# Kernel optimization log

Measured on AMD Instinct MI355X. Metric: run time of the kernel, lower is better.

## Reference

```python
import jax, jax.numpy as jnp
import numpy as np

B, S, D, H = 2, 4096, 128, 128
EPS = 1e-6
NEG_INF = -1e30


def _complex_linear(xr, xi, Wr, Wi, br, bi):
    # x: (B,S,D); W: (H,D); complex linear (Wr + i Wi)(xr + i xi) + (br + i bi) per layer math:
    # real_out = (xr Wr + br) - (xi Wi + bi); imag_out = (xi Wr + br) + (xr Wi + bi)
    out_r = xr @ Wr.T + br - (xi @ Wi.T + bi)
    out_i = xi @ Wr.T + br + (xr @ Wi.T + bi)
    return out_r, out_i


def setup_inputs() -> dict:
    key = jax.random.key(0)
    ks = jax.random.split(key, 24)
    scale = 1.0 / np.sqrt(D)
    def W(k):
        return jax.random.normal(k, (H, D), jnp.float32) * scale
    def b(k):
        return jax.random.normal(k, (H,), jnp.float32) * 0.01
    inp = {
        "Z_q": jax.random.normal(ks[0], (B, 2, S, D, 1), jnp.float32),
        "Z_k": jax.random.normal(ks[1], (B, 2, S, D, 1), jnp.float32),
        "Z_v": jax.random.normal(ks[2], (B, 2, S, D, 1), jnp.float32),
        "Wq_r": W(ks[3]), "Wq_i": W(ks[4]), "bq_r": b(ks[5]), "bq_i": b(ks[6]),
        "Wk_r": W(ks[7]), "Wk_i": W(ks[8]), "bk_r": b(ks[9]), "bk_i": b(ks[10]),
        "Wv_r": W(ks[11]), "Wv_i": W(ks[12]), "bv_r": b(ks[13]), "bv_i": b(ks[14]),
        "Wp_r": W(ks[15]), "Wp_i": W(ks[16]), "bp_r": b(ks[17]), "bp_i": b(ks[18]),
        "noise_floor": jnp.asarray(1.0, jnp.float32),
        "tau": jnp.asarray(0.0, jnp.float32),
    }
    return inp


def reference(Z_q, Z_k, Z_v,
              Wq_r, Wq_i, bq_r, bq_i,
              Wk_r, Wk_i, bk_r, bk_i,
              Wv_r, Wv_i, bv_r, bv_i,
              Wp_r, Wp_i, bp_r, bp_i,
              noise_floor, tau):
    # squeeze trailing singleton; split real/imag -> (B,S,D)
    zqr, zqi = Z_q[:, 0, :, :, 0], Z_q[:, 1, :, :, 0]
    zkr, zki = Z_k[:, 0, :, :, 0], Z_k[:, 1, :, :, 0]
    zvr, zvi = Z_v[:, 0, :, :, 0], Z_v[:, 1, :, :, 0]

    Qr, Qi = _complex_linear(zqr, zqi, Wq_r, Wq_i, bq_r, bq_i)
    Kr, Ki = _complex_linear(zkr, zki, Wk_r, Wk_i, bk_r, bk_i)
    Vr, Vi = _complex_linear(zvr, zvi, Wv_r, Wv_i, bv_r, bv_i)

    # InverseMahalanobis: R2[b,i,j] = sum_h |Q[b,i]-K[b,j]|^2
    q2 = jnp.sum(Qr * Qr + Qi * Qi, axis=-1)          # (B,S)
    k2 = jnp.sum(Kr * Kr + Ki * Ki, axis=-1)          # (B,S)
    re_qk = (jnp.einsum('bsh,bth->bst', Qr, Kr)
             + jnp.einsum('bsh,bth->bst', Qi, Ki))    # (B,S,S)
    R2 = q2[:, :, None] + k2[:, None, :] - 2.0 * re_qk

    attn_scores = -jax.nn.softplus(tau) * jnp.log(noise_floor ** 2 + R2 + EPS)
    mask = jnp.tril(jnp.ones((S, S), dtype=bool))[None]
    attn_scores = jnp.where(mask, attn_scores, NEG_INF)
    attn_weights = jax.nn.softmax(attn_scores / jnp.sqrt(jnp.float32(H)), axis=-1)

    # attn (real) times complex V
    est_r = jnp.einsum('bst,bth->bsh', attn_weights, Vr)
    est_i = jnp.einsum('bst,bth->bsh', attn_weights, Vi)

    out_r, out_i = _complex_linear(est_r, est_i, Wp_r, Wp_i, bp_r, bp_i)
    out = jnp.stack((out_r, out_i), axis=1)[..., None]  # (B,2,S,H,1)
    return out, attn_weights
```

## Files before the change

### kernel.cpp

```cpp
#include <hip/hip_runtime.h>

#define S_LEN 4096
#define OUT_ELEMS 2097152

typedef _Float16 f16;
typedef _Float16 f16x8 __attribute__((ext_vector_type(8)));
typedef _Float16 f16x4 __attribute__((ext_vector_type(4)));
typedef float f32x4 __attribute__((ext_vector_type(4)));

#define MT_OFF    0x000000
#define BIAS_OFF  0x080000
#define SC_OFF    0x081000
#define BVP_OFF   0x082000
#define W2_OFF    0x090000
#define QH_OFF    0x100000
#define KH_OFF    0x500000
#define Q2_OFF    0xD00000
#define K2_OFF    0xD10000
#define L_OFF     0xD20000
#define VPT_OFF   0xE00000
#define PW_OFF    0x1600000
#define WS_NEED   0x5600000

#define MFMA16(A,B,C) __builtin_amdgcn_mfma_f32_16x16x32_f16(A,B,C,0,0,0)

__device__ __forceinline__ void async_cp16(f16* lds, const f16* g) {
  __builtin_amdgcn_global_load_lds(
      (const __attribute__((address_space(1))) void*)g,
      (__attribute__((address_space(3))) void*)lds, 16, 0, 0);
}


__device__ __forceinline__ void stage16(f16* lds, const f16* g, int stride, int tid) {
#pragma unroll
  for (int i = 0; i < 2; ++i) {
    int idx = i*256 + tid;
    int row = idx >> 2, c = idx & 3;
    int cs = c ^ ((row >> 1) & 3);
    async_cp16(lds + idx*8, g + (size_t)row*stride + cs*8);
  }
}

__device__ __forceinline__ void stage32(f16* lds, const float* g, int stride, int tid) {
#pragma unroll
  for (int i = 0; i < 4; ++i) {
    int idx = i*256 + tid;
    int row = idx >> 3, c = idx & 7;
    const float4* gp = (const float4*)(g + (size_t)row*stride + c*4);
    float4 v = *gp;
    f16x4 h; h[0]=(f16)v.x; h[1]=(f16)v.y; h[2]=(f16)v.z; h[3]=(f16)v.w;
    int cl = (((c >> 1) ^ ((row >> 1) & 3)) << 1) | (c & 1);
    *(f16x4*)(lds + row*32 + cl*4) = h;
  }
}

__device__ __forceinline__ void mfma_step(const f16* Asm, const f16* Bsm, int lane,
                                          int wm, int wn, f32x4 acc[4][4]) {
  f16x8 a[4], b[4];
  int rr = lane & 15;
  int sc = (lane >> 4) ^ ((rr >> 1) & 3);
#pragma unroll
  for (int i=0;i<4;i++) a[i] = *(const f16x8*)(Asm + (wm + i*16 + rr)*32 + (sc<<3));
#pragma unroll
  for (int j=0;j<4;j++) b[j] = *(const f16x8*)(Bsm + (wn + j*16 + rr)*32 + (sc<<3));
#pragma unroll
  for (int i=0;i<4;i++)
#pragma unroll
    for (int j=0;j<4;j++) acc[i][j] = MFMA16(a[i], b[j], acc[i][j]);
}

__global__ __launch_bounds__(256)
void k_build(const float* Wqr, const float* Wqi, const float* bqr, const float* bqi,
             const float* Wkr, const float* Wki, const float* bkr, const float* bki,
             const float* Wvr, const float* Wvi, const float* bvr, const float* bvi,
             const float* Wpr, const float* Wpi, const float* bpr, const float* bpi,
             f16* Mt, float* bias) {
  int mat = blockIdx.x;
  const float *Wr, *Wi, *br, *bi;
  if (mat == 0)      { Wr=Wqr; Wi=Wqi; br=bqr; bi=bqi; }
  else if (mat == 1) { Wr=Wkr; Wi=Wki; br=bkr; bi=bki; }
  else if (mat == 2) { Wr=Wvr; Wi=Wvi; br=bvr; bi=bvi; }
  else               { Wr=Wpr; Wi=Wpi; br=bpr; bi=bpi; }
  int idx = blockIdx.y*256 + threadIdx.x;
  int n = idx >> 8, k = idx & 255;
  int d = k & 127, h = n & 127;
  float w = (k < 128) ? ((n < 128) ? Wr[h*128+d] : Wi[h*128+d])
                      : ((n < 128) ? -Wi[h*128+d] : Wr[h*128+d]);
  Mt[mat*65536 + n*256 + k] = (f16)w;
  if (k == 0)
    bias[mat*256 + n] = (n < 128) ? (br[n] - bi[n]) : (br[n-128] + bi[n-128]);
}

__global__ __launch_bounds__(256)
void k_build2(const f16* Mt, const float* bias, f16* W2t, float* bvp) {
  int n = blockIdx.x, k = threadIdx.x;
  const f16* Mtv = Mt + 2*65536;
  const f16* Mtp = Mt + 3*65536;
  float acc = 0.f;
  for (int j = 0; j < 256; ++j)
    acc += (float)Mtv[j*256 + k] * (float)Mtp[n*256 + j];
  W2t[n*256 + k] = (f16)acc;
  if (k == 0) {
    float a = 0.f;
    for (int j = 0; j < 256; ++j) a += bias[2*256 + j] * (float)Mtp[n*256 + j];
    bvp[n] = a;
  }
}

__global__ __launch_bounds__(256)
void k_init(float* outp, float* attn, float* zreg, float* sc, const float* bias,
            const float* nf, const float* tau) {
  int bx = blockIdx.x, tid = threadIdx.x;
  float4 z = make_float4(0.f,0.f,0.f,0.f);
  if (bx < 992) {
    int b = bx >= 496; int r = bx - b*496;
    int tb = 1; while (r >= tb) { r -= tb; tb++; }
    int sb = r;
    float* base = attn + ((size_t)(b*S_LEN) + sb*128)*S_LEN + tb*128;
    int c4 = tid & 31;
#pragma unroll
    for (int it = 0; it < 16; ++it) {
      int row = it*8 + (tid >> 5);
      *(float4*)(base + (size_t)row*S_LEN + c4*4) = z;
    }
    return;
  }
  int idx = (bx - 992)*256 + tid;
  if (idx < 524288) {
    int h4 = idx & 31;
    int comp = (idx >> 17) & 1;
    ((float4*)outp)[idx] = *(const float4*)(bias + 3*256 + comp*128 + h4*4);
  } else {
    int j = idx - 524288;
    if (j < 12288) ((float4*)zreg)[j] = z;
  }
  if (idx == 0) {
    float t = tau[0];
    float c = __builtin_log2f(1.0f + __builtin_exp2f(t * 1.4426950408889634f))
              * 0.6931471805599453f;
    sc[0] = -c * 0.08838834764831845f;
    sc[1] = nf[0]*nf[0] + 1e-6f;
  }
}

__global__ __launch_bounds__(256)
void k_proj(const float* Zq, const float* Zk, const float* Zv,
            const f16* Mt, const f16* W2t, const float* bias, const float* bvp,
            f16* Qh, f16* Kh, f16* VPt, float* q2, float* k2) {
  __shared__ f16 smem[17408];
  __shared__ float bias_s[128];
  f16* A0 = smem;
  f16* A1 = smem + 4096;
  f16* B0 = smem + 8192;
  f16* B1 = smem + 12288;
  int tid = threadIdx.x;
  int mode = blockIdx.z;
  int m0 = blockIdx.x * 128, n0 = blockIdx.y * 128;
  const float* Z = (mode==0) ? Zq : (mode==1 ? Zk : Zv);
  const f16* Bt = (mode==2) ? W2t : (Mt + mode*65536);
  if (tid < 128) bias_s[tid] = (mode==2) ? bvp[n0 + tid] : bias[mode*256 + n0 + tid];
  int b = m0 >> 12, s0 = m0 & 4095;
  int lane = tid & 63, w = tid >> 6;
  int wm = (w >> 1)*64, wn = (w & 1)*64;
  f32x4 acc[4][4] = {};
  {
    const float* Ag = Z + (((size_t)(b*2 + 0))*S_LEN + s0)*128 + 0;
    stage32(A0, Ag, 128, tid);
    stage16(B0, Bt + n0*256 + 0, 256, tid);
  }
  __syncthreads();
  for (int kb = 0; kb < 8; ++kb) {
    int cur = kb & 1;
    if (kb < 7) {
      int k1 = (kb+1)*32;
      int part = k1 >> 7, d0 = k1 & 127;
      const float* Ag = Z + (((size_t)(b*2 + part))*S_LEN + s0)*128 + d0;
      stage32(cur ? A0 : A1, Ag, 128, tid);
      stage16(cur ? B0 : B1, Bt + n0*256 + k1, 256, tid);
    }
    mfma_step(cur ? A1 : A0, cur ? B1 : B0, lane, wm, wn, acc);
    __syncthreads();
  }
  int rr2 = (lane>>4)*4, cc = lane & 15;
  f16* Osm = smem;
  float rs[4][4];
#pragma unroll
  for (int i=0;i<4;i++)
#pragma unroll
    for (int r=0;r<4;r++) rs[i][r]=0.f;
  if (mode < 2) {
#pragma unroll
    for (int i=0;i<4;i++)
#pragma unroll
      for (int j=0;j<4;j++) {
        int cl = wn + j*16 + cc;
        float bv = bias_s[cl];
#pragma unroll
        for (int r=0;r<4;r++) {
          int rl = wm + i*16 + rr2 + r;
          f16 hv = (f16)(acc[i][j][r] + bv);
          Osm[rl*136 + cl] = hv;
          float fv = (float)hv;
          rs[i][r] += fv*fv;
        }
      }
  } else {
#pragma unroll
    for (int i=0;i<4;i++)
#pragma unroll
      for (int j=0;j<4;j++) {
        int cl = wn + j*16 + cc;
        float bv = bias_s[cl];
#pragma unroll
        for (int r=0;r<4;r++) {
          int rl = wm + i*16 + rr2 + r;
          Osm[cl*136 + rl] = (f16)(acc[i][j][r] + bv);
        }
      }
  }
  __syncthreads();
  if (mode < 2) {
    f16* O = (mode==0) ? Qh : Kh;
#pragma unroll
    for (int i2 = 0; i2 < 8; ++i2) {
      int idx = i2*256 + tid;
      int row = idx >> 4, c = idx & 15;
      *(f16x8*)(O + (size_t)(m0+row)*256 + n0 + c*8) = *(const f16x8*)(Osm + row*136 + c*8);
    }
#pragma unroll
    for (int m=8;m>=1;m>>=1)
#pragma unroll
      for (int i=0;i<4;i++)
#pragma unroll
        for (int r=0;r<4;r++) rs[i][r] += __shfl_xor(rs[i][r], m, 64);
    if (cc == 0) {
      float* T = (mode==0) ? q2 : k2;
#pragma unroll
      for (int i=0;i<4;i++)
#pragma unroll
        for (int r=0;r<4;r++) {
          int rg = m0 + wm + i*16 + rr2 + r;
          atomicAdd(&T[rg], rs[i][r]);
        }
    }
  } else {
#pragma unroll
    for (int i2 = 0; i2 < 8; ++i2) {
      int idx = i2*256 + tid;
      int row = idx >> 4, c = idx & 15;
      *(f16x8*)(VPt + (size_t)b*1048576 + (size_t)(n0+row)*4096 + s0 + c*8)
          = *(const f16x8*)(Osm + row*136 + c*8);
    }
  }
}

__global__ __launch_bounds__(256)
void k_attn(const f16* Qh, const f16* Kh, const float* q2, const float* k2,
            const float* sc, float* lsum, f16* Pws) {
  __shared__ f16 smem[4*128*32];
  __shared__ float q2s[128], k2s[128];
  f16* Asm0 = smem;
  f16* Asm1 = smem + 4096;
  f16* Bsm0 = smem + 8192;
  f16* Bsm1 = smem + 12288;
  int x = blockIdx.x;
  int b = x >= 528; int r = x - b*528;
  int sb = 0; while (r > sb) { r -= sb + 1; sb++; }
  int tb = r;
  int s0 = sb*128, t0 = tb*128;
  int tid = threadIdx.x;
  if (tid < 128) {
    q2s[tid] = q2[b*S_LEN + s0 + tid];
    k2s[tid] = k2[b*S_LEN + t0 + tid];
  }
  float kc = sc[0], nf2 = sc[1];
  int lane = tid & 63, w = tid >> 6;
  int wm = (w >> 1)*64, wn = (w & 1)*64;
  const f16* Ag = Qh + ((size_t)(b*S_LEN) + s0)*256;
  const f16* Bg = Kh + ((size_t)(b*S_LEN) + t0)*256;
  f32x4 acc[4][4] = {};
  stage16(Asm0, Ag, 256, tid);
  stage16(Bsm0, Bg, 256, tid);
  __syncthreads();
  for (int kb=0;kb<8;kb++) {
    int cur = kb & 1;
    if (kb < 7) {
      stage16(cur ? Asm0 : Asm1, Ag + (kb+1)*32, 256, tid);
      stage16(cur ? Bsm0 : Bsm1, Bg + (kb+1)*32, 256, tid);
    }
    mfma_step(cur ? Asm1 : Asm0, cur ? Bsm1 : Bsm0, lane, wm, wn, acc);
    __syncthreads();
  }
  f16* Psm = smem;
  int rr = (lane>>4)*4, cc = lane & 15;
  bool diag = (tb == sb);
  float rs[4][4];
#pragma unroll
  for (int i=0;i<4;i++)
#pragma unroll
    for (int rg=0;rg<4;rg++) rs[i][rg]=0.f;
#pragma unroll
  for (int i=0;i<4;i++)
#pragma unroll
    for (int j=0;j<4;j++) {
      int cl = wn + j*16 + cc;
      float kv = k2s[cl];
#pragma unroll
      for (int rg=0;rg<4;rg++) {
        int rl = wm + i*16 + rr + rg;
        float xx = nf2 + q2s[rl] + kv - 2.0f*acc[i][j][rg];
        float P = __builtin_exp2f(kc * __builtin_log2f(__builtin_fmaxf(xx, 1e-6f)));
        if (diag && (t0+cl) > (s0+rl)) P = 0.f;
        Psm[rl*128 + cl] = (f16)P;
        rs[i][rg] += P;
      }
    }
  __syncthreads();
  f16* Pg = Pws + ((size_t)(b*S_LEN) + s0)*S_LEN + t0;
#pragma unroll
  for (int i2 = 0; i2 < 8; ++i2) {
    int idx = i2*256 + tid;
    int row = idx >> 4, c = idx & 15;
    *(f16x8*)(Pg + (size_t)row*S_LEN + c*8) = *(const f16x8*)(Psm + row*128 + c*8);
  }
#pragma unroll
  for (int m=8;m>=1;m>>=1)
#pragma unroll
    for (int i=0;i<4;i++)
#pragma unroll
      for (int rg=0;rg<4;rg++) rs[i][rg] += __shfl_xor(rs[i][rg], m, 64);
  if (cc == 0)
#pragma unroll
    for (int i=0;i<4;i++)
#pragma unroll
      for (int rg=0;rg<4;rg++) {
        int rl = wm + i*16 + rr + rg;
        atomicAdd(&lsum[b*S_LEN + s0 + rl], rs[i][rg]);
      }
}

__global__ __launch_bounds__(512)
void k_pv(const f16* Pws, const f16* VPt, const float* lsum, float* outp, float* attn) {
  __shared__ f16 Asm[2][128*32];
  __shared__ f16 Bsm[2][256*32];
  __shared__ float ls[128];
  int r = blockIdx.x, b = blockIdx.y;
  int sb = 0;
  while (r >= ((sb+4)>>2)) { r -= (sb+4)>>2; sb++; }
  int c = r;
  int s0 = sb*128;
  int tid = threadIdx.x;
  if (tid < 128) ls[tid] = 1.0f / lsum[b*S_LEN + s0 + tid];
  int lane = tid & 63, w = tid >> 6;
  int wm = (w>>2)*64, wn = (w&3)*64;
  int tb0 = c*4, tb1 = tb0 + 4; if (tb1 > sb+1) tb1 = sb+1;
  int nt = (tb1 - tb0) * 4;
  int base_t = tb0*128;
  const f16* Abase = Pws + ((size_t)(b*S_LEN) + s0)*S_LEN + base_t;
  const f16* Bbase = VPt + (size_t)b*1048576 + base_t;
  f32x4 acc[4][4] = {};
  {
    int row = tid >> 2, cc0 = tid & 3, cs = cc0 ^ ((row >> 1) & 3);
    async_cp16(Asm[0] + tid*8, Abase + (size_t)row*S_LEN + cs*8);
  }
#pragma unroll
  for (int i=0;i<2;i++) {
    int idx = i*512 + tid, row = idx >> 2, cc0 = idx & 3, cs = cc0 ^ ((row >> 1) & 3);
    async_cp16(Bsm[0] + idx*8, Bbase + (size_t)row*4096 + cs*8);
  }
  __syncthreads();
  for (int st = 0; st < nt; ++st) {
    int cur = st & 1;
    int tcur = base_t + st*32;
    if (st + 1 < nt) {
      const f16* Ag = Abase + (st+1)*32;
      const f16* Bg = Bbase + (st+1)*32;
      {
        int row = tid >> 2, cc0 = tid & 3, cs = cc0 ^ ((row >> 1) & 3);
        async_cp16(Asm[cur^1] + tid*8, Ag + (size_t)row*S_LEN + cs*8);
      }
#pragma unroll
      for (int i=0;i<2;i++) {
        int idx = i*512 + tid, row = idx >> 2, cc0 = idx & 3, cs = cc0 ^ ((row >> 1) & 3);
        async_cp16(Bsm[cur^1] + idx*8, Bg + (size_t)row*4096 + cs*8);
      }
    }
#pragma unroll
    for (int i2=0;i2<2;i2++) {
      int idx = i2*512 + tid, row = idx >> 3, c4 = idx & 7;
      int cs = (c4 >> 1) ^ ((row >> 1) & 3);
      f16x4 v = *(const f16x4*)(Asm[cur] + row*32 + cs*8 + (c4 & 1)*4);
      float invl = ls[row];
      float4 o;
      o.x=(float)v[0]*invl; o.y=(float)v[1]*invl;
      o.z=(float)v[2]*invl; o.w=(float)v[3]*invl;
      *(float4*)(attn + ((size_t)(b*S_LEN) + s0 + row)*S_LEN + tcur + c4*4) = o;
    }
    mfma_step(Asm[cur], Bsm[cur], lane, wm, wn, acc);
    __syncthreads();
  }
  int rr2 = (lane>>4)*4, cc = lane & 15;
#pragma unroll
  for (int i=0;i<4;i++)
#pragma unroll
    for (int j=0;j<4;j++) {
      int cg = wn + j*16 + cc;
      int comp = cg >> 7, h = cg & 127;
#pragma unroll
      for (int rg=0;rg<4;rg++) {
        int rl = wm + i*16 + rr2 + rg;
        float v = acc[i][j][rg] * ls[rl];
        atomicAdd(&outp[(((size_t)(b*2 + comp))*S_LEN + s0 + rl)*128 + h], v);
      }
    }
}

extern "C" void kernel_launch(void* const* d_in, const int* in_sizes, int n_in,
                              void* d_out, int out_size, void* d_ws, size_t ws_size,
                              hipStream_t stream) {
  (void)in_sizes; (void)n_in; (void)out_size;
  if (ws_size < (size_t)WS_NEED) return;
  const float* Zq = (const float*)d_in[0];
  const float* Zk = (const float*)d_in[1];
  const float* Zv = (const float*)d_in[2];
  char* ws = (char*)d_ws;
  f16*   Mt   = (f16*)(ws + MT_OFF);
  float* bias = (float*)(ws + BIAS_OFF);
  float* sc   = (float*)(ws + SC_OFF);
  float* bvp  = (float*)(ws + BVP_OFF);
  f16*   W2t  = (f16*)(ws + W2_OFF);
  f16*   Qh   = (f16*)(ws + QH_OFF);
  f16*   Kh   = (f16*)(ws + KH_OFF);
  float* q2   = (float*)(ws + Q2_OFF);
  float* k2   = (float*)(ws + K2_OFF);
  float* lsum = (float*)(ws + L_OFF);
  f16*   VPt  = (f16*)(ws + VPT_OFF);
  f16*   Pws  = (f16*)(ws + PW_OFF);
  float* outp = (float*)d_out;
  float* attn = outp + OUT_ELEMS;

  k_build<<<dim3(4,256), 256, 0, stream>>>(
      (const float*)d_in[3],  (const float*)d_in[4],  (const float*)d_in[5],  (const float*)d_in[6],
      (const float*)d_in[7],  (const float*)d_in[8],  (const float*)d_in[9],  (const float*)d_in[10],
      (const float*)d_in[11], (const float*)d_in[12], (const float*)d_in[13], (const float*)d_in[14],
      (const float*)d_in[15], (const float*)d_in[16], (const float*)d_in[17], (const float*)d_in[18],
      Mt, bias);
  k_build2<<<256, 256, 0, stream>>>(Mt, bias, W2t, bvp);
  k_init<<<3088, 256, 0, stream>>>(outp, attn, q2, sc, bias,
                                   (const float*)d_in[19], (const float*)d_in[20]);
  k_proj<<<dim3(64,2,3), 256, 0, stream>>>(Zq, Zk, Zv, Mt, W2t, bias, bvp,
                                           Qh, Kh, VPt, q2, k2);
  k_attn<<<1056, 256, 0, stream>>>(Qh, Kh, q2, k2, sc, lsum, Pws);
  k_pv<<<dim3(144,2), 512, 0, stream>>>(Pws, VPt, lsum, outp, attn);
}
```

Baseline: 303.2 us.

## Prefetch two stages ahead with explicit vmcnt waits in score and PV kernels

Both MFMA main loops now issue async global-to-LDS copies two k-steps ahead instead of one. __syncthreads is replaced by explicit s_waitcnt vmcnt counts, raw s_barrier calls and sched_barrier fences, so a load can remain in flight while the previous tile is consumed. The aim is to hide global memory latency behind MFMA work. The hand-counted vmcnt values depend on the exact number of memory instructions the compiler emits (including the attn stores in the PV loop), which risks races if the counts are wrong.

```diff
diff --git a/kernel.cpp b/kernel.cpp
--- a/kernel.cpp
+++ b/kernel.cpp
@@ -279,17 +279,26 @@
   const f16* Ag = Qh + ((size_t)(b*S_LEN) + s0)*256;
   const f16* Bg = Kh + ((size_t)(b*S_LEN) + t0)*256;
   f32x4 acc[4][4] = {};
-  stage16(Asm0, Ag, 256, tid);
-  stage16(Bsm0, Bg, 256, tid);
-  __syncthreads();
-  for (int kb=0;kb<8;kb++) {
-    int cur = kb & 1;
-    if (kb < 7) {
-      stage16(cur ? Asm0 : Asm1, Ag + (kb+1)*32, 256, tid);
-      stage16(cur ? Bsm0 : Bsm1, Bg + (kb+1)*32, 256, tid);
-    }
-    mfma_step(cur ? Asm1 : Asm0, cur ? Bsm1 : Bsm0, lane, wm, wn, acc);
-    __syncthreads();
+  stage16(Asm0, Ag,      256, tid);
+  stage16(Bsm0, Bg,      256, tid);
+  stage16(Asm1, Ag + 32, 256, tid);
+  stage16(Bsm1, Bg + 32, 256, tid);
+  for (int kb = 0; kb < 8; ++kb) {
+    if (kb == 0)      asm volatile("s_waitcnt vmcnt(4) lgkmcnt(0)" ::: "memory");
+    else if (kb == 7) asm volatile("s_waitcnt vmcnt(0)" ::: "memory");
+    else              asm volatile("s_waitcnt vmcnt(4)" ::: "memory");
+    __builtin_amdgcn_s_barrier();
+    __builtin_amdgcn_sched_barrier(0);
+    f16* Acur = (kb & 1) ? Asm1 : Asm0;
+    f16* Bcur = (kb & 1) ? Bsm1 : Bsm0;
+    mfma_step(Acur, Bcur, lane, wm, wn, acc);
+    __builtin_amdgcn_sched_barrier(0);
+    __builtin_amdgcn_s_barrier();
+    __builtin_amdgcn_sched_barrier(0);
+    if (kb < 6) {
+      stage16(Acur, Ag + (kb+2)*32, 256, tid);
+      stage16(Bcur, Bg + (kb+2)*32, 256, tid);
+    }
   }
   f16* Psm = smem;
   int rr = (lane>>4)*4, cc = lane & 15;
@@ -359,32 +368,24 @@
   const f16* Abase = Pws + ((size_t)(b*S_LEN) + s0)*S_LEN + base_t;
   const f16* Bbase = VPt + (size_t)b*1048576 + base_t;
   f32x4 acc[4][4] = {};
-  {
-    int row = tid >> 2, cc0 = tid & 3, cs = cc0 ^ ((row >> 1) & 3);
-    async_cp16(Asm[0] + tid*8, Abase + (size_t)row*S_LEN + cs*8);
-  }
-#pragma unroll
-  for (int i=0;i<2;i++) {
-    int idx = i*512 + tid, row = idx >> 2, cc0 = idx & 3, cs = cc0 ^ ((row >> 1) & 3);
-    async_cp16(Bsm[0] + idx*8, Bbase + (size_t)row*4096 + cs*8);
-  }
-  __syncthreads();
+  int rowA = tid >> 2, ccA = tid & 3, csA = ccA ^ ((rowA >> 1) & 3);
+#pragma unroll
+  for (int t = 0; t < 2; ++t) {
+    async_cp16(Asm[t] + tid*8, Abase + t*32 + (size_t)rowA*S_LEN + csA*8);
+#pragma unroll
+    for (int i=0;i<2;i++) {
+      int idx = i*512 + tid, row = idx >> 2, cc0 = idx & 3, cs = cc0 ^ ((row >> 1) & 3);
+      async_cp16(Bsm[t] + idx*8, Bbase + t*32 + (size_t)row*4096 + cs*8);
+    }
+  }
   for (int st = 0; st < nt; ++st) {
     int cur = st & 1;
     int tcur = base_t + st*32;
-    if (st + 1 < nt) {
-      const f16* Ag = Abase + (st+1)*32;
-      const f16* Bg = Bbase + (st+1)*32;
-      {
-        int row = tid >> 2, cc0 = tid & 3, cs = cc0 ^ ((row >> 1) & 3);
-        async_cp16(Asm[cur^1] + tid*8, Ag + (size_t)row*S_LEN + cs*8);
-      }
-#pragma unroll
-      for (int i=0;i<2;i++) {
-        int idx = i*512 + tid, row = idx >> 2, cc0 = idx & 3, cs = cc0 ^ ((row >> 1) & 3);
-        async_cp16(Bsm[cur^1] + idx*8, Bg + (size_t)row*4096 + cs*8);
-      }
-    }
+    if (st == 0)           asm volatile("s_waitcnt vmcnt(3) lgkmcnt(0)" ::: "memory");
+    else if (st == nt - 1) asm volatile("s_waitcnt vmcnt(2)" ::: "memory");
+    else                   asm volatile("s_waitcnt vmcnt(5)" ::: "memory");
+    __builtin_amdgcn_s_barrier();
+    __builtin_amdgcn_sched_barrier(0);
 #pragma unroll
     for (int i2=0;i2<2;i2++) {
       int idx = i2*512 + tid, row = idx >> 3, c4 = idx & 7;
@@ -397,7 +398,19 @@
       *(float4*)(attn + ((size_t)(b*S_LEN) + s0 + row)*S_LEN + tcur + c4*4) = o;
     }
     mfma_step(Asm[cur], Bsm[cur], lane, wm, wn, acc);
-    __syncthreads();
+    __builtin_amdgcn_sched_barrier(0);
+    __builtin_amdgcn_s_barrier();
+    __builtin_amdgcn_sched_barrier(0);
+    if (st + 2 < nt) {
+      const f16* Ag = Abase + (st+2)*32;
+      const f16* Bg = Bbase + (st+2)*32;
+      async_cp16(Asm[cur] + tid*8, Ag + (size_t)rowA*S_LEN + csA*8);
+#pragma unroll
+      for (int i=0;i<2;i++) {
+        int idx = i*512 + tid, row = idx >> 2, cc0 = idx & 3, cs = cc0 ^ ((row >> 1) & 3);
+        async_cp16(Bsm[cur] + idx*8, Bg + (size_t)row*4096 + cs*8);
+      }
+    }
   }
   int rr2 = (lane>>4)*4, cc = lane & 15;
 #pragma unroll
```

After: 316.0 us. 4.2% more time.
